# Optimization experiments

Measured on AMD Instinct MI355X. Metric: run time of the kernel, lower is better.

Reference implementation:

```python
import jax, jax.numpy as jnp
import numpy as np

N = 50000
E = 800000
IN = 256
OUT = 32
H1 = 8
NEG_SLOPE = 0.2


def setup_inputs() -> dict:
    key = jax.random.key(0)
    ks = jax.random.split(key, 12)
    x = jax.random.normal(ks[0], (N, IN), dtype=jnp.float32)
    src = jax.random.randint(ks[1], (E,), 0, N, dtype=jnp.int32)
    dst = jax.random.randint(ks[2], (E,), 0, N, dtype=jnp.int32)
    s1 = 1.0 / np.sqrt(IN)
    s2 = 1.0 / np.sqrt(H1 * OUT)
    # layer 1 (8 heads, residual = Identity since IN == H1*OUT)
    W1 = jax.random.normal(ks[3], (IN, H1 * OUT), dtype=jnp.float32) * s1
    al1 = jax.random.normal(ks[4], (H1, OUT), dtype=jnp.float32) * s1
    ar1 = jax.random.normal(ks[5], (H1, OUT), dtype=jnp.float32) * s1
    b1 = jnp.zeros((H1 * OUT,), dtype=jnp.float32)
    # layer 2 (1 head, residual = Linear since H1*OUT != OUT)
    W2 = jax.random.normal(ks[6], (H1 * OUT, OUT), dtype=jnp.float32) * s2
    al2 = jax.random.normal(ks[7], (1, OUT), dtype=jnp.float32) * s2
    ar2 = jax.random.normal(ks[8], (1, OUT), dtype=jnp.float32) * s2
    resW2 = jax.random.normal(ks[9], (H1 * OUT, OUT), dtype=jnp.float32) * s2
    b2 = jnp.zeros((OUT,), dtype=jnp.float32)
    return {"x": x, "src": src, "dst": dst, "W1": W1, "al1": al1, "ar1": ar1,
            "b1": b1, "W2": W2, "al2": al2, "ar2": ar2, "resW2": resW2, "b2": b2}


def gat_layer(x, src, dst, W, al, ar, bias, heads, out_feats, res_fn):
    # x: (N, in). feat: (N, H, D)
    feat = (x @ W).reshape(N, heads, out_feats)
    el = jnp.sum(feat * al[None], axis=-1)  # (N, H)
    er = jnp.sum(feat * ar[None], axis=-1)  # (N, H)
    e = jax.nn.leaky_relu(el[src] + er[dst], NEG_SLOPE)  # (E, H)
    # edge softmax over incoming edges of each destination node
    emax = jax.ops.segment_max(e, dst, num_segments=N)  # (N, H)
    ee = jnp.exp(e - emax[dst])
    esum = jax.ops.segment_sum(ee, dst, num_segments=N)  # (N, H)
    a = ee / esum[dst]  # (E, H)
    # gather-multiply-scatter-add aggregation
    msg = feat[src] * a[..., None]  # (E, H, D)
    rst = jax.ops.segment_sum(msg, dst, num_segments=N)  # (N, H, D)
    rst = rst + res_fn(x)
    rst = rst + bias.reshape(1, heads, out_feats)
    return rst


def reference(x, src, dst, W1, al1, ar1, b1, W2, al2, ar2, resW2, b2):
    # layer 1: 8 heads, residual Identity (IN == H1*OUT)
    y = gat_layer(x, src, dst, W1, al1, ar1, b1, H1, OUT,
                  lambda h: h.reshape(N, H1, OUT))
    y = jax.nn.relu(y).reshape(N, H1 * OUT)
    # layer 2: 1 head, residual Linear projection
    y = gat_layer(y, src, dst, W2, al2, ar2, b2, 1, OUT,
                  lambda h: (h @ resW2).reshape(N, 1, OUT))
    return y
```

## Files before the change

kernel.cpp:

```cpp
#include <hip/hip_runtime.h>
#include <hip/hip_bf16.h>
#include <hip/hip_fp8.h>

#define N_NODES 50000
#define M_PAD   50048
#define N_EDGES 800000
#define NEG_SLOPE 0.2f

#define SCAN_BLK 256
#define SCAN_NB ((N_NODES + SCAN_BLK - 1) / SCAN_BLK)
#define EPT 8
#define HIST_BLOCKS 391
#define GHALF 782
#define MEGA_T (HIST_BLOCKS + GHALF)
#define MEGA_PRIME 577ull

typedef __attribute__((ext_vector_type(8))) short bf16x8;
typedef __attribute__((ext_vector_type(4))) float f32x4;
typedef __attribute__((ext_vector_type(2))) float f32x2;

__device__ __forceinline__ unsigned short f2bf(float f) {
    unsigned u = __float_as_uint(f);
    u += 0x7FFFu + ((u >> 16) & 1u);
    return (unsigned short)(u >> 16);
}
__device__ __forceinline__ float bf2f(unsigned short h) {
    return __uint_as_float(((unsigned)h) << 16);
}

#if __has_builtin(__builtin_amdgcn_cvt_pk_f32_fp8)
__device__ __forceinline__ f32x2 fp8pk_lo(unsigned int p) { return __builtin_amdgcn_cvt_pk_f32_fp8(p, false); }
__device__ __forceinline__ f32x2 fp8pk_hi(unsigned int p) { return __builtin_amdgcn_cvt_pk_f32_fp8(p, true); }
#else
__device__ __forceinline__ float fp82f_s(unsigned char b) {
    __hip_fp8_e4m3 t; t.__x = (__hip_fp8_storage_t)b; return (float)t;
}
__device__ __forceinline__ f32x2 fp8pk_lo(unsigned int p) {
    f32x2 r; r.x = fp82f_s(p & 0xff); r.y = fp82f_s((p >> 8) & 0xff); return r;
}
__device__ __forceinline__ f32x2 fp8pk_hi(unsigned int p) {
    f32x2 r; r.x = fp82f_s((p >> 16) & 0xff); r.y = fp82f_s(p >> 24); return r;
}
#endif

#if __has_builtin(__builtin_amdgcn_cvt_pk_fp8_f32)
__device__ __forceinline__ unsigned int fp8enc2(float a, float b) {
    return (unsigned int)__builtin_amdgcn_cvt_pk_fp8_f32(a, b, 0, false);
}
#else
__device__ __forceinline__ unsigned int fp8enc2(float a, float b) {
    __hip_fp8_e4m3 ta(a), tb(b);
    return (unsigned int)ta.__x | ((unsigned int)tb.__x << 8);
}
#endif


__global__ __launch_bounds__(256) void k_trans(const float* __restrict__ W1, const float* __restrict__ W2,
                                               const float* __restrict__ resW2, const float* __restrict__ x,
                                               unsigned short* __restrict__ W1T, unsigned short* __restrict__ W2T,
                                               unsigned short* __restrict__ xb, int* __restrict__ deg) {
    int flat = blockIdx.y * 10 + blockIdx.x;
    for (int i = flat * 256 + threadIdx.x; i < N_NODES; i += 800 * 256) deg[i] = 0;

    if (blockIdx.y < 8) {
        __shared__ unsigned short tile[32][33];
        int bx = blockIdx.x;
        const float* in;
        unsigned short* out;
        int Nn, n0;
        if (bx < 8)      { in = W1;    out = W1T;            Nn = 256; n0 = bx * 32; }
        else if (bx == 8){ in = W2;    out = W2T;            Nn = 32;  n0 = 0; }
        else             { in = resW2; out = W2T + 32 * 256; Nn = 32;  n0 = 0; }
        int k0 = blockIdx.y * 32;
        int tx = threadIdx.x & 31, ty = threadIdx.x >> 5;
        #pragma unroll
        for (int r = 0; r < 4; ++r) {
            int k = k0 + ty + r * 8;
            tile[ty + r * 8][tx] = f2bf(in[(size_t)k * Nn + n0 + tx]);
        }
        __syncthreads();
        #pragma unroll
        for (int r = 0; r < 4; ++r) {
            int n = ty + r * 8;
            out[(size_t)(n0 + n) * 256 + k0 + tx] = tile[tx][n];
        }
    } else {
        int xid = flat - 80;
        const size_t NCHUNK = (size_t)M_PAD * 256 / 8;
        for (size_t c = (size_t)xid * 256 + threadIdx.x; c < NCHUNK; c += (size_t)720 * 256) {
            size_t base = c * 8;
            float4 a = make_float4(0.f, 0.f, 0.f, 0.f), b = a;
            if (base < (size_t)N_NODES * 256) {
                a = *(const float4*)(x + base);
                b = *(const float4*)(x + base + 4);
            }
            ushort4 h0, h1;
            h0.x = f2bf(a.x); h0.y = f2bf(a.y); h0.z = f2bf(a.z); h0.w = f2bf(a.w);
            h1.x = f2bf(b.x); h1.y = f2bf(b.y); h1.z = f2bf(b.z); h1.w = f2bf(b.w);
            *(ushort4*)(xb + base) = h0;
            *(ushort4*)(xb + base + 4) = h1;
        }
    }
}


__device__ __forceinline__ void gemm1_half(int g, int bn0,
                                           const unsigned short* __restrict__ xb,
                                           const unsigned short* __restrict__ BT,
                                           const float* __restrict__ al1, const float* __restrict__ ar1,
                                           unsigned char* __restrict__ Cb8,
                                           float* __restrict__ el1, float* __restrict__ er1) {
    const int t = threadIdx.x;
    const int bm0 = g * 64;
    const int wave = t >> 6, lane = t & 63;
    const int wm = (wave & 1) * 32, wn = (wave >> 1) * 64;
    const int lm = lane & 15, quad = lane >> 4;

    f32x4 acc[2][4];
    #pragma unroll
    for (int i = 0; i < 2; ++i)
        #pragma unroll
        for (int j = 0; j < 4; ++j)
            #pragma unroll
            for (int r = 0; r < 4; ++r) acc[i][j][r] = 0.f;

    const unsigned short* bp[4];
    const unsigned short* ap[2];
    #pragma unroll
    for (int i = 0; i < 4; ++i)
        bp[i] = BT + (size_t)(bn0 + wn + i * 16 + lm) * 256 + quad * 8;
    #pragma unroll
    for (int i = 0; i < 2; ++i)
        ap[i] = xb + (size_t)(bm0 + wm + i * 16 + lm) * 256 + quad * 8;

    bf16x8 nb[4], na[2];
    #pragma unroll
    for (int i = 0; i < 4; ++i) nb[i] = *(const bf16x8*)(bp[i]);
    #pragma unroll
    for (int i = 0; i < 2; ++i) na[i] = *(const bf16x8*)(ap[i]);

    #pragma unroll
    for (int k0 = 0; k0 < 256; k0 += 32) {
        bf16x8 cb[4], ca[2];
        #pragma unroll
        for (int i = 0; i < 4; ++i) cb[i] = nb[i];
        #pragma unroll
        for (int i = 0; i < 2; ++i) ca[i] = na[i];
        if (k0 + 32 < 256) {
            #pragma unroll
            for (int i = 0; i < 4; ++i) nb[i] = *(const bf16x8*)(bp[i] + k0 + 32);
            #pragma unroll
            for (int i = 0; i < 2; ++i) na[i] = *(const bf16x8*)(ap[i] + k0 + 32);
        }
        #pragma unroll
        for (int mi = 0; mi < 2; ++mi)
            #pragma unroll
            for (int ni = 0; ni < 4; ++ni)
                acc[mi][ni] = __builtin_amdgcn_mfma_f32_16x16x32_bf16(ca[mi], cb[ni], acc[mi][ni], 0, 0, 0);
    }

    #pragma unroll
    for (int mi = 0; mi < 2; ++mi) {
        #pragma unroll
        for (int ni = 0; ni < 4; ++ni) {
            int col = bn0 + wn + ni * 16 + lm;
            int row0 = bm0 + wm + mi * 16 + quad * 4;
            unsigned int p01 = fp8enc2(acc[mi][ni][0], acc[mi][ni][1]);
            unsigned int p23 = fp8enc2(acc[mi][ni][2], acc[mi][ni][3]);
            Cb8[(size_t)(row0 + 0) * 256 + col] = (unsigned char)(p01 & 0xff);
            Cb8[(size_t)(row0 + 1) * 256 + col] = (unsigned char)((p01 >> 8) & 0xff);
            Cb8[(size_t)(row0 + 2) * 256 + col] = (unsigned char)(p23 & 0xff);
            Cb8[(size_t)(row0 + 3) * 256 + col] = (unsigned char)((p23 >> 8) & 0xff);
        }
    }
    float alv[4], arv[4];
    #pragma unroll
    for (int ni = 0; ni < 4; ++ni) {
        int colg = bn0 + wn + ni * 16 + lm;
        alv[ni] = al1[colg];
        arv[ni] = ar1[colg];
    }
    int head0 = (bn0 + wn) >> 5;
    #pragma unroll
    for (int gg = 0; gg < 2; ++gg) {
        #pragma unroll
        for (int mi = 0; mi < 2; ++mi) {
            #pragma unroll
            for (int r = 0; r < 4; ++r) {
                float pel = acc[mi][2 * gg][r] * alv[2 * gg] + acc[mi][2 * gg + 1][r] * alv[2 * gg + 1];
                float per = acc[mi][2 * gg][r] * arv[2 * gg] + acc[mi][2 * gg + 1][r] * arv[2 * gg + 1];
                #pragma unroll
                for (int m = 1; m <= 8; m <<= 1) {
                    pel += __shfl_xor(pel, m, 64);
                    per += __shfl_xor(per, m, 64);
                }
                if (lm == 0) {
                    int row = bm0 + wm + mi * 16 + quad * 4 + r;
                    el1[row * 8 + head0 + gg] = pel;
                    er1[row * 8 + head0 + gg] = per;
                }
            }
        }
    }
}


__global__ __launch_bounds__(256) void k_mega1(const int* __restrict__ dst, int* __restrict__ deg,
                                               int* __restrict__ rank,
                                               const unsigned short* __restrict__ xb,
                                               const unsigned short* __restrict__ BT,
                                               const float* __restrict__ al1, const float* __restrict__ ar1,
                                               unsigned char* __restrict__ Cb8,
                                               float* __restrict__ el1, float* __restrict__ er1) {
    unsigned vb = (unsigned)(((unsigned long long)blockIdx.x * MEGA_PRIME) % MEGA_T);
    if (vb < HIST_BLOCKS) {
        int base = vb * (256 * EPT) + threadIdx.x;
        int dv[EPT];
        #pragma unroll
        for (int q = 0; q < EPT; ++q) {
            int i = base + q * 256;
            dv[q] = (i < N_EDGES) ? dst[i] : -1;
        }
        #pragma unroll
        for (int q = 0; q < EPT; ++q) {
            if (dv[q] >= 0) rank[base + q * 256] = atomicAdd(&deg[dv[q]], 1);
        }
        return;
    }
    gemm1_half(vb - HIST_BLOCKS, 0, xb, BT, al1, ar1, Cb8, el1, er1);
}


__global__ __launch_bounds__(256) void k_mega2(const int* __restrict__ src, const int* __restrict__ dst,
                                               const int* __restrict__ rowoff, const int* __restrict__ rank,
                                               int* __restrict__ csr_src,
                                               const unsigned short* __restrict__ xb,
                                               const unsigned short* __restrict__ BT,
                                               const float* __restrict__ al1, const float* __restrict__ ar1,
                                               unsigned char* __restrict__ Cb8,
                                               float* __restrict__ el1, float* __restrict__ er1) {
    unsigned vb = (unsigned)(((unsigned long long)blockIdx.x * MEGA_PRIME) % MEGA_T);
    if (vb < HIST_BLOCKS) {
        int base = vb * (256 * EPT) + threadIdx.x;
        int sv[EPT], dv[EPT], rk[EPT];
        #pragma unroll
        for (int q = 0; q < EPT; ++q) {
            int i = base + q * 256;
            if (i < N_EDGES) { sv[q] = src[i]; dv[q] = dst[i]; rk[q] = rank[i]; }
            else dv[q] = -1;
        }
        int ro[EPT];
        #pragma unroll
        for (int q = 0; q < EPT; ++q) {
            if (dv[q] >= 0) ro[q] = rowoff[dv[q]];
        }
        #pragma unroll
        for (int q = 0; q < EPT; ++q) {
            if (dv[q] >= 0) csr_src[ro[q] + rk[q]] = sv[q];
        }
        return;
    }
    gemm1_half(vb - HIST_BLOCKS, 128, xb, BT, al1, ar1, Cb8, el1, er1);
}


__global__ __launch_bounds__(SCAN_BLK) void k_scan1(const int* __restrict__ deg,
                                                    int* __restrict__ rowoff,
                                                    int* __restrict__ bsum) {
    __shared__ int s[SCAN_BLK];
    int i = blockIdx.x * SCAN_BLK + threadIdx.x;
    int v = (i < N_NODES) ? deg[i] : 0;
    s[threadIdx.x] = v;
    __syncthreads();
    for (int off = 1; off < SCAN_BLK; off <<= 1) {
        int t = (threadIdx.x >= off) ? s[threadIdx.x - off] : 0;
        __syncthreads();
        s[threadIdx.x] += t;
        __syncthreads();
    }
    if (i < N_NODES) rowoff[i] = s[threadIdx.x];
    if (threadIdx.x == SCAN_BLK - 1) bsum[blockIdx.x] = s[SCAN_BLK - 1];
}

__global__ __launch_bounds__(SCAN_BLK) void k_scan3(const int* __restrict__ deg,
                                                    int* __restrict__ rowoff,
                                                    const int* __restrict__ bsum) {
    __shared__ int red[4];
    int t = threadIdx.x;
    int part = 0;
    for (int i = t; i < (int)blockIdx.x; i += SCAN_BLK) part += bsum[i];
    #pragma unroll
    for (int m = 1; m <= 32; m <<= 1) part += __shfl_xor(part, m, 64);
    if ((t & 63) == 0) red[t >> 6] = part;
    __syncthreads();
    if (t == 0) red[0] = red[0] + red[1] + red[2] + red[3];
    __syncthreads();
    int off = red[0];
    int i = blockIdx.x * SCAN_BLK + t;
    if (i < N_NODES) rowoff[i] = rowoff[i] - deg[i] + off;
    if (i == 0) rowoff[N_NODES] = N_EDGES;
}


__global__ __launch_bounds__(256) void k_agg1(const unsigned char* __restrict__ feat8,
                                              const float* __restrict__ el1, const float* __restrict__ er1,
                                              const unsigned short* __restrict__ xb, const float* __restrict__ b1,
                                              const int* __restrict__ rowoff, const int* __restrict__ csr_src,
                                              unsigned short* __restrict__ y_b) {
    int v = (blockIdx.x * 256 + threadIdx.x) >> 6;
    int lane = threadIdx.x & 63;
    if (v >= M_PAD) return;
    int c0 = lane * 4;
    if (v >= N_NODES) {
        ushort4 z = {0, 0, 0, 0};
        *(ushort4*)(y_b + (size_t)v * 256 + c0) = z;
        return;
    }
    int h = lane >> 3;
    float er = er1[v * 8 + h];
    float ax = 0.f, ay = 0.f, az = 0.f, aw = 0.f, wsum = 0.f;
    int s = rowoff[v], e = rowoff[v + 1];
    int j = s;
    for (; j + 7 < e; j += 8) {
        int u[8];
        #pragma unroll
        for (int q = 0; q < 8; ++q) u[q] = csr_src[j + q];
        float tt[8];
        #pragma unroll
        for (int q = 0; q < 8; ++q) tt[q] = el1[u[q] * 8 + h] + er;
        unsigned int hv[8];
        #pragma unroll
        for (int q = 0; q < 8; ++q) hv[q] = *(const unsigned int*)(feat8 + (size_t)u[q] * 256 + c0);
        #pragma unroll
        for (int q = 0; q < 8; ++q) {
            float tq = tt[q] > 0.f ? tt[q] : NEG_SLOPE * tt[q];
            float w = __expf(tq);
            wsum += w;
            f32x2 lo = fp8pk_lo(hv[q]);
            f32x2 hi = fp8pk_hi(hv[q]);
            ax += w * lo.x; ay += w * lo.y; az += w * hi.x; aw += w * hi.y;
        }
    }
    for (; j + 3 < e; j += 4) {
        int u[4];
        #pragma unroll
        for (int q = 0; q < 4; ++q) u[q] = csr_src[j + q];
        float tt[4];
        #pragma unroll
        for (int q = 0; q < 4; ++q) tt[q] = el1[u[q] * 8 + h] + er;
        unsigned int hv[4];
        #pragma unroll
        for (int q = 0; q < 4; ++q) hv[q] = *(const unsigned int*)(feat8 + (size_t)u[q] * 256 + c0);
        #pragma unroll
        for (int q = 0; q < 4; ++q) {
            float tq = tt[q] > 0.f ? tt[q] : NEG_SLOPE * tt[q];
            float w = __expf(tq);
            wsum += w;
            f32x2 lo = fp8pk_lo(hv[q]);
            f32x2 hi = fp8pk_hi(hv[q]);
            ax += w * lo.x; ay += w * lo.y; az += w * hi.x; aw += w * hi.y;
        }
    }
    for (; j < e; ++j) {
        int u = csr_src[j];
        float t = el1[u * 8 + h] + er;
        unsigned int hh = *(const unsigned int*)(feat8 + (size_t)u * 256 + c0);
        t = t > 0.f ? t : NEG_SLOPE * t;
        float w = __expf(t);
        wsum += w;
        f32x2 lo = fp8pk_lo(hh);
        f32x2 hi = fp8pk_hi(hh);
        ax += w * lo.x; ay += w * lo.y; az += w * hi.x; aw += w * hi.y;
    }
    float inv = (e > s) ? 1.f / wsum : 0.f;
    ushort4 rh = *(const ushort4*)(xb + (size_t)v * 256 + c0);
    float4 bb = *(const float4*)(b1 + c0);
    ushort4 o;
    o.x = f2bf(fmaxf(ax * inv + bf2f(rh.x) + bb.x, 0.f));
    o.y = f2bf(fmaxf(ay * inv + bf2f(rh.y) + bb.y, 0.f));
    o.z = f2bf(fmaxf(az * inv + bf2f(rh.z) + bb.z, 0.f));
    o.w = f2bf(fmaxf(aw * inv + bf2f(rh.w) + bb.w, 0.f));
    *(ushort4*)(y_b + (size_t)v * 256 + c0) = o;
}


__global__ __launch_bounds__(256) void k_gemm2f(const unsigned short* __restrict__ Ab,
                                                const unsigned short* __restrict__ BT,
                                                const float* __restrict__ al2, const float* __restrict__ ar2,
                                                unsigned short* __restrict__ feat2b, float* __restrict__ res2,
                                                float* __restrict__ el2, float* __restrict__ er2) {
    const int t = threadIdx.x;
    const int bm0 = blockIdx.x * 64;
    const int wave = t >> 6, lane = t & 63;
    const int wm = (wave & 1) * 32, wn = (wave >> 1) * 32;
    const int lm = lane & 15, quad = lane >> 4;

    f32x4 acc[2][2];
    #pragma unroll
    for (int i = 0; i < 2; ++i)
        #pragma unroll
        for (int j = 0; j < 2; ++j)
            #pragma unroll
            for (int r = 0; r < 4; ++r) acc[i][j][r] = 0.f;

    const unsigned short* bp[2];
    const unsigned short* ap[2];
    #pragma unroll
    for (int i = 0; i < 2; ++i) {
        bp[i] = BT + (size_t)(wn + i * 16 + lm) * 256 + quad * 8;
        ap[i] = Ab + (size_t)(bm0 + wm + i * 16 + lm) * 256 + quad * 8;
    }

    bf16x8 nb[2], na[2];
    #pragma unroll
    for (int i = 0; i < 2; ++i) { nb[i] = *(const bf16x8*)(bp[i]); na[i] = *(const bf16x8*)(ap[i]); }

    #pragma unroll
    for (int k0 = 0; k0 < 256; k0 += 32) {
        bf16x8 cb[2], ca[2];
        #pragma unroll
        for (int i = 0; i < 2; ++i) { cb[i] = nb[i]; ca[i] = na[i]; }
        if (k0 + 32 < 256) {
            #pragma unroll
            for (int i = 0; i < 2; ++i) {
                nb[i] = *(const bf16x8*)(bp[i] + k0 + 32);
                na[i] = *(const bf16x8*)(ap[i] + k0 + 32);
            }
        }
        #pragma unroll
        for (int mi = 0; mi < 2; ++mi)
            #pragma unroll
            for (int ni = 0; ni < 2; ++ni)
                acc[mi][ni] = __builtin_amdgcn_mfma_f32_16x16x32_bf16(ca[mi], cb[ni], acc[mi][ni], 0, 0, 0);
    }

    #pragma unroll
    for (int mi = 0; mi < 2; ++mi) {
        #pragma unroll
        for (int ni = 0; ni < 2; ++ni) {
            int col = wn + ni * 16 + lm;
            #pragma unroll
            for (int r = 0; r < 4; ++r) {
                int row = bm0 + wm + mi * 16 + quad * 4 + r;
                float val = acc[mi][ni][r];
                if (col < 32) feat2b[(size_t)row * 32 + col] = f2bf(val);
                else          res2[(size_t)row * 32 + col - 32] = val;
            }
        }
    }
    if (wn == 0) {
        float alv[2], arv[2];
        #pragma unroll
        for (int ni = 0; ni < 2; ++ni) {
            alv[ni] = al2[ni * 16 + lm];
            arv[ni] = ar2[ni * 16 + lm];
        }
        #pragma unroll
        for (int mi = 0; mi < 2; ++mi) {
            #pragma unroll
            for (int r = 0; r < 4; ++r) {
                float pel = acc[mi][0][r] * alv[0] + acc[mi][1][r] * alv[1];
                float per = acc[mi][0][r] * arv[0] + acc[mi][1][r] * arv[1];
                #pragma unroll
                for (int m = 1; m <= 8; m <<= 1) {
                    pel += __shfl_xor(pel, m, 64);
                    per += __shfl_xor(per, m, 64);
                }
                if (lm == 0) {
                    int row = bm0 + wm + mi * 16 + quad * 4 + r;
                    el2[row] = pel;
                    er2[row] = per;
                }
            }
        }
    }
}


__global__ __launch_bounds__(256) void k_agg2(const unsigned short* __restrict__ feat2b,
                                              const float* __restrict__ el2, const float* __restrict__ er2,
                                              const float* __restrict__ res2, const float* __restrict__ b2,
                                              const int* __restrict__ rowoff, const int* __restrict__ csr_src,
                                              float* __restrict__ out) {
    int g = blockIdx.x * 256 + threadIdx.x;
    int v = g >> 5;
    int c = g & 31;
    if (v >= N_NODES) return;
    float er = er2[v];
    float acc = 0.f, wsum = 0.f;
    int s = rowoff[v], e = rowoff[v + 1];
    int j = s;
    for (; j + 3 < e; j += 4) {
        int u[4];
        #pragma unroll
        for (int q = 0; q < 4; ++q) u[q] = csr_src[j + q];
        float tt[4];
        #pragma unroll
        for (int q = 0; q < 4; ++q) tt[q] = el2[u[q]] + er;
        unsigned short fv[4];
        #pragma unroll
        for (int q = 0; q < 4; ++q) fv[q] = feat2b[(size_t)u[q] * 32 + c];
        #pragma unroll
        for (int q = 0; q < 4; ++q) {
            float tq = tt[q] > 0.f ? tt[q] : NEG_SLOPE * tt[q];
            float w = __expf(tq);
            wsum += w;
            acc += w * bf2f(fv[q]);
        }
    }
    for (; j < e; ++j) {
        int u = csr_src[j];
        float t = el2[u] + er;
        t = t > 0.f ? t : NEG_SLOPE * t;
        float w = __expf(t);
        wsum += w;
        acc += w * bf2f(feat2b[(size_t)u * 32 + c]);
    }
    float inv = (e > s) ? 1.f / wsum : 0.f;
    out[(size_t)v * 32 + c] = acc * inv + res2[(size_t)v * 32 + c] + b2[c];
}


extern "C" void kernel_launch(void* const* d_in, const int* in_sizes, int n_in,
                              void* d_out, int out_size, void* d_ws, size_t ws_size,
                              hipStream_t stream) {
    const float* x     = (const float*)d_in[0];
    const int*   src   = (const int*)d_in[1];
    const int*   dst   = (const int*)d_in[2];
    const float* W1    = (const float*)d_in[3];
    const float* al1   = (const float*)d_in[4];
    const float* ar1   = (const float*)d_in[5];
    const float* b1    = (const float*)d_in[6];
    const float* W2    = (const float*)d_in[7];
    const float* al2   = (const float*)d_in[8];
    const float* ar2   = (const float*)d_in[9];
    const float* resW2 = (const float*)d_in[10];
    const float* b2    = (const float*)d_in[11];
    float* out = (float*)d_out;

    char* ws = (char*)d_ws;
    size_t off = 0;
    auto alloc = [&](size_t bytes) {
        void* p = ws + off;
        off += (bytes + 255) & ~(size_t)255;
        return p;
    };
    unsigned short* xb     = (unsigned short*)alloc((size_t)M_PAD * 256 * 2);
    unsigned char*  feat8  = (unsigned char*)alloc((size_t)M_PAD * 256);
    unsigned short* y_b    = (unsigned short*)alloc((size_t)M_PAD * 256 * 2);
    unsigned short* W1T    = (unsigned short*)alloc((size_t)256 * 256 * 2);
    unsigned short* W2T    = (unsigned short*)alloc((size_t)64 * 256 * 2);
    unsigned short* feat2b = (unsigned short*)alloc((size_t)M_PAD * 32 * 2);
    float* res2   = (float*)alloc((size_t)M_PAD * 32 * 4);
    float* el1    = (float*)alloc((size_t)M_PAD * 8 * 4);
    float* er1    = (float*)alloc((size_t)M_PAD * 8 * 4);
    float* el2    = (float*)alloc((size_t)M_PAD * 4);
    float* er2    = (float*)alloc((size_t)M_PAD * 4);
    int*   deg    = (int*)alloc((size_t)N_NODES * 4);
    int*   rank   = (int*)alloc((size_t)N_EDGES * 4);
    int*   rowoff = (int*)alloc((size_t)(N_NODES + 1) * 4);
    int*   bsum   = (int*)alloc((size_t)SCAN_NB * 4);
    int*   csr    = (int*)alloc((size_t)N_EDGES * 4);
    (void)ws_size;

    k_trans<<<dim3(10, 80), 256, 0, stream>>>(W1, W2, resW2, x, W1T, W2T, xb, deg);

    k_mega1<<<MEGA_T, 256, 0, stream>>>(dst, deg, rank, xb, W1T, al1, ar1, feat8, el1, er1);

    k_scan1<<<SCAN_NB, SCAN_BLK, 0, stream>>>(deg, rowoff, bsum);
    k_scan3<<<SCAN_NB, SCAN_BLK, 0, stream>>>(deg, rowoff, bsum);

    k_mega2<<<MEGA_T, 256, 0, stream>>>(src, dst, rowoff, rank, csr, xb, W1T, al1, ar1, feat8, el1, er1);

    k_agg1<<<(M_PAD * 64) / 256, 256, 0, stream>>>(feat8, el1, er1, xb, b1, rowoff, csr, y_b);

    k_gemm2f<<<M_PAD / 64, 256, 0, stream>>>(y_b, W2T, al2, ar2, feat2b, res2, el2, er2);
    k_agg2<<<(N_NODES * 32) / 256, 256, 0, stream>>>(feat2b, el2, er2, res2, b2, rowoff, csr, out);
}
```

Measured before the change: 280.2 us.

## Split GEMM1 into 64-column tiles and share edge weights across lanes in aggregation

```diff
diff --git a/kernel.cpp b/kernel.cpp
--- a/kernel.cpp
+++ b/kernel.cpp
@@ -11,9 +11,9 @@
 #define SCAN_NB ((N_NODES + SCAN_BLK - 1) / SCAN_BLK)
 #define EPT 8
 #define HIST_BLOCKS 391
-#define GHALF 782
-#define MEGA_T (HIST_BLOCKS + GHALF)
-#define MEGA_PRIME 577ull
+#define GEMM_BLOCKS 1564
+#define MEGA_T (HIST_BLOCKS + GEMM_BLOCKS)
+#define MEGA_PRIME 997ull
 
 typedef __attribute__((ext_vector_type(8))) short bf16x8;
 typedef __attribute__((ext_vector_type(4))) float f32x4;
@@ -104,65 +104,61 @@
 }
 
 
-__device__ __forceinline__ void gemm1_half(int g, int bn0,
-                                           const unsigned short* __restrict__ xb,
-                                           const unsigned short* __restrict__ BT,
-                                           const float* __restrict__ al1, const float* __restrict__ ar1,
-                                           unsigned char* __restrict__ Cb8,
-                                           float* __restrict__ el1, float* __restrict__ er1) {
+__device__ __forceinline__ void gemm1_64(int gm, int bn0,
+                                         const unsigned short* __restrict__ xb,
+                                         const unsigned short* __restrict__ BT,
+                                         const float* __restrict__ al1, const float* __restrict__ ar1,
+                                         unsigned char* __restrict__ Cb8,
+                                         float* __restrict__ el1, float* __restrict__ er1) {
     const int t = threadIdx.x;
-    const int bm0 = g * 64;
+    const int bm0 = gm * 64;
     const int wave = t >> 6, lane = t & 63;
-    const int wm = (wave & 1) * 32, wn = (wave >> 1) * 64;
+    const int wm = (wave & 1) * 32, wn = (wave >> 1) * 32;
     const int lm = lane & 15, quad = lane >> 4;
 
-    f32x4 acc[2][4];
+    f32x4 acc[2][2];
     #pragma unroll
     for (int i = 0; i < 2; ++i)
         #pragma unroll
-        for (int j = 0; j < 4; ++j)
+        for (int j = 0; j < 2; ++j)
             #pragma unroll
             for (int r = 0; r < 4; ++r) acc[i][j][r] = 0.f;
 
-    const unsigned short* bp[4];
+    const unsigned short* bp[2];
     const unsigned short* ap[2];
     #pragma unroll
-    for (int i = 0; i < 4; ++i)
+    for (int i = 0; i < 2; ++i) {
         bp[i] = BT + (size_t)(bn0 + wn + i * 16 + lm) * 256 + quad * 8;
-    #pragma unroll
-    for (int i = 0; i < 2; ++i)
         ap[i] = xb + (size_t)(bm0 + wm + i * 16 + lm) * 256 + quad * 8;
-
-    bf16x8 nb[4], na[2];
-    #pragma unroll
-    for (int i = 0; i < 4; ++i) nb[i] = *(const bf16x8*)(bp[i]);
-    #pragma unroll
-    for (int i = 0; i < 2; ++i) na[i] = *(const bf16x8*)(ap[i]);
+    }
+
+    bf16x8 nb[2], na[2];
+    #pragma unroll
+    for (int i = 0; i < 2; ++i) { nb[i] = *(const bf16x8*)(bp[i]); na[i] = *(const bf16x8*)(ap[i]); }
 
     #pragma unroll
     for (int k0 = 0; k0 < 256; k0 += 32) {
-        bf16x8 cb[4], ca[2];
-        #pragma unroll
-        for (int i = 0; i < 4; ++i) cb[i] = nb[i];
-        #pragma unroll
-        for (int i = 0; i < 2; ++i) ca[i] = na[i];
+        bf16x8 cb[2], ca[2];
+        #pragma unroll
+        for (int i = 0; i < 2; ++i) { cb[i] = nb[i]; ca[i] = na[i]; }
         if (k0 + 32 < 256) {
             #pragma unroll
-            for (int i = 0; i < 4; ++i) nb[i] = *(const bf16x8*)(bp[i] + k0 + 32);
-            #pragma unroll
-            for (int i = 0; i < 2; ++i) na[i] = *(const bf16x8*)(ap[i] + k0 + 32);
+            for (int i = 0; i < 2; ++i) {
+                nb[i] = *(const bf16x8*)(bp[i] + k0 + 32);
+                na[i] = *(const bf16x8*)(ap[i] + k0 + 32);
+            }
         }
         #pragma unroll
         for (int mi = 0; mi < 2; ++mi)
             #pragma unroll
-            for (int ni = 0; ni < 4; ++ni)
+            for (int ni = 0; ni < 2; ++ni)
                 acc[mi][ni] = __builtin_amdgcn_mfma_f32_16x16x32_bf16(ca[mi], cb[ni], acc[mi][ni], 0, 0, 0);
     }
 
     #pragma unroll
     for (int mi = 0; mi < 2; ++mi) {
         #pragma unroll
-        for (int ni = 0; ni < 4; ++ni) {
+        for (int ni = 0; ni < 2; ++ni) {
             int col = bn0 + wn + ni * 16 + lm;
             int row0 = bm0 + wm + mi * 16 + quad * 4;
             unsigned int p01 = fp8enc2(acc[mi][ni][0], acc[mi][ni][1]);
@@ -173,32 +169,29 @@
             Cb8[(size_t)(row0 + 3) * 256 + col] = (unsigned char)((p23 >> 8) & 0xff);
         }
     }
-    float alv[4], arv[4];
-    #pragma unroll
-    for (int ni = 0; ni < 4; ++ni) {
+    int head = (bn0 + wn) >> 5;
+    float alv[2], arv[2];
+    #pragma unroll
+    for (int ni = 0; ni < 2; ++ni) {
         int colg = bn0 + wn + ni * 16 + lm;
         alv[ni] = al1[colg];
         arv[ni] = ar1[colg];
     }
-    int head0 = (bn0 + wn) >> 5;
-    #pragma unroll
-    for (int gg = 0; gg < 2; ++gg) {
-        #pragma unroll
-        for (int mi = 0; mi < 2; ++mi) {
-            #pragma unroll
-            for (int r = 0; r < 4; ++r) {
-                float pel = acc[mi][2 * gg][r] * alv[2 * gg] + acc[mi][2 * gg + 1][r] * alv[2 * gg + 1];
-                float per = acc[mi][2 * gg][r] * arv[2 * gg] + acc[mi][2 * gg + 1][r] * arv[2 * gg + 1];
-                #pragma unroll
-                for (int m = 1; m <= 8; m <<= 1) {
-                    pel += __shfl_xor(pel, m, 64);
-                    per += __shfl_xor(per, m, 64);
-                }
-                if (lm == 0) {
-                    int row = bm0 + wm + mi * 16 + quad * 4 + r;
-                    el1[row * 8 + head0 + gg] = pel;
-                    er1[row * 8 + head0 + gg] = per;
-                }
+    #pragma unroll
+    for (int mi = 0; mi < 2; ++mi) {
+        #pragma unroll
+        for (int r = 0; r < 4; ++r) {
+            float pel = acc[mi][0][r] * alv[0] + acc[mi][1][r] * alv[1];
+            float per = acc[mi][0][r] * arv[0] + acc[mi][1][r] * arv[1];
+            #pragma unroll
+            for (int m = 1; m <= 8; m <<= 1) {
+                pel += __shfl_xor(pel, m, 64);
+                per += __shfl_xor(per, m, 64);
+            }
+            if (lm == 0) {
+                int row = bm0 + wm + mi * 16 + quad * 4 + r;
+                el1[row * 8 + head] = pel;
+                er1[row * 8 + head] = per;
             }
         }
     }
@@ -227,7 +220,8 @@
         }
         return;
     }
-    gemm1_half(vb - HIST_BLOCKS, 0, xb, BT, al1, ar1, Cb8, el1, er1);
+    int g = vb - HIST_BLOCKS;
+    gemm1_64(g >> 1, (g & 1) * 64, xb, BT, al1, ar1, Cb8, el1, er1);
 }
 
 
@@ -260,7 +254,8 @@
         }
         return;
     }
-    gemm1_half(vb - HIST_BLOCKS, 128, xb, BT, al1, ar1, Cb8, el1, er1);
+    int g = vb - HIST_BLOCKS;
+    gemm1_64(g >> 1, 128 + (g & 1) * 64, xb, BT, al1, ar1, Cb8, el1, er1);
 }
 
 
@@ -317,23 +312,45 @@
         return;
     }
     int h = lane >> 3;
-    float er = er1[v * 8 + h];
+    float er  = er1[v * 8 + h];
+    float erc = er1[v * 8 + (lane & 7)];
     float ax = 0.f, ay = 0.f, az = 0.f, aw = 0.f, wsum = 0.f;
     int s = rowoff[v], e = rowoff[v + 1];
     int j = s;
     for (; j + 7 < e; j += 8) {
+        int um = csr_src[j + (lane >> 3)];
+        float elv = el1[um * 8 + (lane & 7)];
         int u[8];
         #pragma unroll
-        for (int q = 0; q < 8; ++q) u[q] = csr_src[j + q];
-        float tt[8];
-        #pragma unroll
-        for (int q = 0; q < 8; ++q) tt[q] = el1[u[q] * 8 + h] + er;
+        for (int q = 0; q < 8; ++q) u[q] = __shfl(um, q * 8);
         unsigned int hv[8];
         #pragma unroll
         for (int q = 0; q < 8; ++q) hv[q] = *(const unsigned int*)(feat8 + (size_t)u[q] * 256 + c0);
+        float tq = elv + erc;
+        tq = fmaxf(tq, NEG_SLOPE * tq);
+        float wv = __expf(tq);
         #pragma unroll
         for (int q = 0; q < 8; ++q) {
-            float tq = tt[q] > 0.f ? tt[q] : NEG_SLOPE * tt[q];
+            float w = __shfl(wv, q * 8 + h);
+            wsum += w;
+            f32x2 lo = fp8pk_lo(hv[q]);
+            f32x2 hi = fp8pk_hi(hv[q]);
+            ax += w * lo.x; ay += w * lo.y; az += w * hi.x; aw += w * hi.y;
+        }
+    }
+    for (; j + 3 < e; j += 4) {
+        int u[4];
+        #pragma unroll
+        for (int q = 0; q < 4; ++q) u[q] = csr_src[j + q];
+        float tt[4];
+        #pragma unroll
+        for (int q = 0; q < 4; ++q) tt[q] = el1[u[q] * 8 + h] + er;
+        unsigned int hv[4];
+        #pragma unroll
+        for (int q = 0; q < 4; ++q) hv[q] = *(const unsigned int*)(feat8 + (size_t)u[q] * 256 + c0);
+        #pragma unroll
+        for (int q = 0; q < 4; ++q) {
+            float tq = fmaxf(tt[q], NEG_SLOPE * tt[q]);
             float w = __expf(tq);
             wsum += w;
             f32x2 lo = fp8pk_lo(hv[q]);
@@ -341,31 +358,11 @@
             ax += w * lo.x; ay += w * lo.y; az += w * hi.x; aw += w * hi.y;
         }
     }
-    for (; j + 3 < e; j += 4) {
-        int u[4];
-        #pragma unroll
-        for (int q = 0; q < 4; ++q) u[q] = csr_src[j + q];
-        float tt[4];
-        #pragma unroll
-        for (int q = 0; q < 4; ++q) tt[q] = el1[u[q] * 8 + h] + er;
-        unsigned int hv[4];
-        #pragma unroll
-        for (int q = 0; q < 4; ++q) hv[q] = *(const unsigned int*)(feat8 + (size_t)u[q] * 256 + c0);
-        #pragma unroll
-        for (int q = 0; q < 4; ++q) {
-            float tq = tt[q] > 0.f ? tt[q] : NEG_SLOPE * tt[q];
-            float w = __expf(tq);
-            wsum += w;
-            f32x2 lo = fp8pk_lo(hv[q]);
-            f32x2 hi = fp8pk_hi(hv[q]);
-            ax += w * lo.x; ay += w * lo.y; az += w * hi.x; aw += w * hi.y;
-        }
-    }
     for (; j < e; ++j) {
         int u = csr_src[j];
         float t = el1[u * 8 + h] + er;
         unsigned int hh = *(const unsigned int*)(feat8 + (size_t)u * 256 + c0);
-        t = t > 0.f ? t : NEG_SLOPE * t;
+        t = fmaxf(t, NEG_SLOPE * t);
         float w = __expf(t);
         wsum += w;
         f32x2 lo = fp8pk_lo(hh);
@@ -502,7 +499,7 @@
         for (int q = 0; q < 4; ++q) fv[q] = feat2b[(size_t)u[q] * 32 + c];
         #pragma unroll
         for (int q = 0; q < 4; ++q) {
-            float tq = tt[q] > 0.f ? tt[q] : NEG_SLOPE * tt[q];
+            float tq = fmaxf(tt[q], NEG_SLOPE * tt[q]);
             float w = __expf(tq);
             wsum += w;
             acc += w * bf2f(fv[q]);
@@ -511,7 +508,7 @@
     for (; j < e; ++j) {
         int u = csr_src[j];
         float t = el2[u] + er;
-        t = t > 0.f ? t : NEG_SLOPE * t;
+        t = fmaxf(t, NEG_SLOPE * t);
         float w = __expf(t);
         wsum += w;
         acc += w * bf2f(feat2b[(size_t)u * 32 + c]);
```

Result: slower. 287.9 us (+2.8%).

## Build CSR via bucketed shared-memory counting sort, drop scan kernels

Applied to the files above, without the earlier changes.

```diff
diff --git a/kernel.cpp b/kernel.cpp
--- a/kernel.cpp
+++ b/kernel.cpp
@@ -7,13 +7,16 @@
 #define N_EDGES 800000
 #define NEG_SLOPE 0.2f
 
-#define SCAN_BLK 256
-#define SCAN_NB ((N_NODES + SCAN_BLK - 1) / SCAN_BLK)
 #define EPT 8
-#define HIST_BLOCKS 391
+#define BKA 391
+#define NBUCK 256
+#define NPB 196
+#define SEGCAP 40
 #define GHALF 782
-#define MEGA_T (HIST_BLOCKS + GHALF)
-#define MEGA_PRIME 577ull
+#define MEGA1_T (BKA + GHALF)
+#define MEGA1_PRIME 577ull
+#define MEGA2_T (NBUCK + GHALF)
+#define MEGA2_PRIME 521ull
 
 typedef __attribute__((ext_vector_type(8))) short bf16x8;
 typedef __attribute__((ext_vector_type(4))) float f32x4;
@@ -58,9 +61,9 @@
 __global__ __launch_bounds__(256) void k_trans(const float* __restrict__ W1, const float* __restrict__ W2,
                                                const float* __restrict__ resW2, const float* __restrict__ x,
                                                unsigned short* __restrict__ W1T, unsigned short* __restrict__ W2T,
-                                               unsigned short* __restrict__ xb, int* __restrict__ deg) {
+                                               unsigned short* __restrict__ xb, unsigned int* __restrict__ btot) {
     int flat = blockIdx.y * 10 + blockIdx.x;
-    for (int i = flat * 256 + threadIdx.x; i < N_NODES; i += 800 * 256) deg[i] = 0;
+    if (flat == 0) btot[threadIdx.x] = 0;
 
     if (blockIdx.y < 8) {
         __shared__ unsigned short tile[32][33];
@@ -205,100 +208,111 @@
 }
 
 
-__global__ __launch_bounds__(256) void k_mega1(const int* __restrict__ dst, int* __restrict__ deg,
-                                               int* __restrict__ rank,
+__global__ __launch_bounds__(256) void k_mega1(const int* __restrict__ src, const int* __restrict__ dst,
+                                               uint2* __restrict__ seg, unsigned int* __restrict__ cnt,
+                                               unsigned int* __restrict__ btot,
                                                const unsigned short* __restrict__ xb,
                                                const unsigned short* __restrict__ BT,
                                                const float* __restrict__ al1, const float* __restrict__ ar1,
                                                unsigned char* __restrict__ Cb8,
                                                float* __restrict__ el1, float* __restrict__ er1) {
-    unsigned vb = (unsigned)(((unsigned long long)blockIdx.x * MEGA_PRIME) % MEGA_T);
-    if (vb < HIST_BLOCKS) {
+    __shared__ unsigned int lcnt[NBUCK];
+    unsigned vb = (unsigned)(((unsigned long long)blockIdx.x * MEGA1_PRIME) % MEGA1_T);
+    if (vb < BKA) {
+        lcnt[threadIdx.x] = 0;
+        __syncthreads();
         int base = vb * (256 * EPT) + threadIdx.x;
-        int dv[EPT];
+        int sv[EPT], dv[EPT], bk[EPT], lr[EPT];
         #pragma unroll
         for (int q = 0; q < EPT; ++q) {
             int i = base + q * 256;
-            dv[q] = (i < N_EDGES) ? dst[i] : -1;
+            if (i < N_EDGES) { sv[q] = src[i]; dv[q] = dst[i]; }
+            else dv[q] = -1;
         }
         #pragma unroll
         for (int q = 0; q < EPT; ++q) {
-            if (dv[q] >= 0) rank[base + q * 256] = atomicAdd(&deg[dv[q]], 1);
+            if (dv[q] >= 0) {
+                bk[q] = (int)((unsigned)dv[q] / NPB);
+                lr[q] = atomicAdd(&lcnt[bk[q]], 1u);
+            }
+        }
+        __syncthreads();
+        cnt[vb * NBUCK + threadIdx.x] = lcnt[threadIdx.x];
+        if (lcnt[threadIdx.x] > 0) atomicAdd(&btot[threadIdx.x], lcnt[threadIdx.x]);
+        #pragma unroll
+        for (int q = 0; q < EPT; ++q) {
+            if (dv[q] >= 0 && lr[q] < SEGCAP) {
+                size_t slot = ((size_t)bk[q] * BKA + vb) * SEGCAP + lr[q];
+                seg[slot] = make_uint2((unsigned)sv[q], (unsigned)dv[q] - (unsigned)bk[q] * NPB);
+            }
         }
         return;
     }
-    gemm1_half(vb - HIST_BLOCKS, 0, xb, BT, al1, ar1, Cb8, el1, er1);
-}
-
-
-__global__ __launch_bounds__(256) void k_mega2(const int* __restrict__ src, const int* __restrict__ dst,
-                                               const int* __restrict__ rowoff, const int* __restrict__ rank,
-                                               int* __restrict__ csr_src,
+    gemm1_half(vb - BKA, 0, xb, BT, al1, ar1, Cb8, el1, er1);
+}
+
+
+__global__ __launch_bounds__(256) void k_mega2(const uint2* __restrict__ seg, const unsigned int* __restrict__ cnt,
+                                               const unsigned int* __restrict__ btot,
+                                               int* __restrict__ rowoff, int* __restrict__ csr_src,
                                                const unsigned short* __restrict__ xb,
                                                const unsigned short* __restrict__ BT,
                                                const float* __restrict__ al1, const float* __restrict__ ar1,
                                                unsigned char* __restrict__ Cb8,
                                                float* __restrict__ el1, float* __restrict__ er1) {
-    unsigned vb = (unsigned)(((unsigned long long)blockIdx.x * MEGA_PRIME) % MEGA_T);
-    if (vb < HIST_BLOCKS) {
-        int base = vb * (256 * EPT) + threadIdx.x;
-        int sv[EPT], dv[EPT], rk[EPT];
-        #pragma unroll
-        for (int q = 0; q < EPT; ++q) {
-            int i = base + q * 256;
-            if (i < N_EDGES) { sv[q] = src[i]; dv[q] = dst[i]; rk[q] = rank[i]; }
-            else dv[q] = -1;
-        }
-        int ro[EPT];
-        #pragma unroll
-        for (int q = 0; q < EPT; ++q) {
-            if (dv[q] >= 0) ro[q] = rowoff[dv[q]];
-        }
-        #pragma unroll
-        for (int q = 0; q < EPT; ++q) {
-            if (dv[q] >= 0) csr_src[ro[q] + rk[q]] = sv[q];
+    __shared__ unsigned int hist[NPB];
+    __shared__ unsigned int cursor[NPB];
+    __shared__ unsigned int red[256];
+    unsigned vb = (unsigned)(((unsigned long long)blockIdx.x * MEGA2_PRIME) % MEGA2_T);
+    if (vb < NBUCK) {
+        int b = (int)vb;
+        int t = threadIdx.x;
+        if (t < NPB) hist[t] = 0;
+        red[t] = (t < b) ? btot[t] : 0;
+        __syncthreads();
+        #pragma unroll
+        for (int off = 128; off > 0; off >>= 1) {
+            if (t < off) red[t] += red[t + off];
+            __syncthreads();
+        }
+        unsigned int base = red[0];
+        __syncthreads();
+        for (int s = t; s < BKA; s += 256) {
+            unsigned int c = cnt[s * NBUCK + b];
+            const uint2* sp = seg + ((size_t)b * BKA + s) * SEGCAP;
+            for (unsigned int j = 0; j < c; ++j) {
+                atomicAdd(&hist[sp[j].y], 1u);
+            }
+        }
+        __syncthreads();
+        red[t] = (t < NPB) ? hist[t] : 0;
+        __syncthreads();
+        for (int off = 1; off < 256; off <<= 1) {
+            unsigned int val = (t >= off) ? red[t - off] : 0;
+            __syncthreads();
+            red[t] += val;
+            __syncthreads();
+        }
+        if (t < NPB) {
+            unsigned int excl = red[t] - hist[t];
+            cursor[t] = excl;
+            int v = b * NPB + t;
+            if (v < N_NODES) rowoff[v] = (int)(base + excl);
+        }
+        if (b == NBUCK - 1 && t == 0) rowoff[N_NODES] = N_EDGES;
+        __syncthreads();
+        for (int s = t; s < BKA; s += 256) {
+            unsigned int c = cnt[s * NBUCK + b];
+            const uint2* sp = seg + ((size_t)b * BKA + s) * SEGCAP;
+            for (unsigned int j = 0; j < c; ++j) {
+                uint2 eg = sp[j];
+                unsigned int r = atomicAdd(&cursor[eg.y], 1u);
+                csr_src[base + r] = (int)eg.x;
+            }
         }
         return;
     }
-    gemm1_half(vb - HIST_BLOCKS, 128, xb, BT, al1, ar1, Cb8, el1, er1);
-}
-
-
-__global__ __launch_bounds__(SCAN_BLK) void k_scan1(const int* __restrict__ deg,
-                                                    int* __restrict__ rowoff,
-                                                    int* __restrict__ bsum) {
-    __shared__ int s[SCAN_BLK];
-    int i = blockIdx.x * SCAN_BLK + threadIdx.x;
-    int v = (i < N_NODES) ? deg[i] : 0;
-    s[threadIdx.x] = v;
-    __syncthreads();
-    for (int off = 1; off < SCAN_BLK; off <<= 1) {
-        int t = (threadIdx.x >= off) ? s[threadIdx.x - off] : 0;
-        __syncthreads();
-        s[threadIdx.x] += t;
-        __syncthreads();
-    }
-    if (i < N_NODES) rowoff[i] = s[threadIdx.x];
-    if (threadIdx.x == SCAN_BLK - 1) bsum[blockIdx.x] = s[SCAN_BLK - 1];
-}
-
-__global__ __launch_bounds__(SCAN_BLK) void k_scan3(const int* __restrict__ deg,
-                                                    int* __restrict__ rowoff,
-                                                    const int* __restrict__ bsum) {
-    __shared__ int red[4];
-    int t = threadIdx.x;
-    int part = 0;
-    for (int i = t; i < (int)blockIdx.x; i += SCAN_BLK) part += bsum[i];
-    #pragma unroll
-    for (int m = 1; m <= 32; m <<= 1) part += __shfl_xor(part, m, 64);
-    if ((t & 63) == 0) red[t >> 6] = part;
-    __syncthreads();
-    if (t == 0) red[0] = red[0] + red[1] + red[2] + red[3];
-    __syncthreads();
-    int off = red[0];
-    int i = blockIdx.x * SCAN_BLK + t;
-    if (i < N_NODES) rowoff[i] = rowoff[i] - deg[i] + off;
-    if (i == 0) rowoff[N_NODES] = N_EDGES;
+    gemm1_half(vb - NBUCK, 128, xb, BT, al1, ar1, Cb8, el1, er1);
 }
 
 
@@ -317,23 +331,45 @@
         return;
     }
     int h = lane >> 3;
-    float er = er1[v * 8 + h];
+    float er  = er1[v * 8 + h];
+    float erc = er1[v * 8 + (lane & 7)];
     float ax = 0.f, ay = 0.f, az = 0.f, aw = 0.f, wsum = 0.f;
     int s = rowoff[v], e = rowoff[v + 1];
     int j = s;
     for (; j + 7 < e; j += 8) {
+        int um = csr_src[j + (lane >> 3)];
+        float elv = el1[um * 8 + (lane & 7)];
         int u[8];
         #pragma unroll
-        for (int q = 0; q < 8; ++q) u[q] = csr_src[j + q];
-        float tt[8];
-        #pragma unroll
-        for (int q = 0; q < 8; ++q) tt[q] = el1[u[q] * 8 + h] + er;
+        for (int q = 0; q < 8; ++q) u[q] = __shfl(um, q * 8);
         unsigned int hv[8];
         #pragma unroll
         for (int q = 0; q < 8; ++q) hv[q] = *(const unsigned int*)(feat8 + (size_t)u[q] * 256 + c0);
+        float tq = elv + erc;
+        tq = fmaxf(tq, NEG_SLOPE * tq);
+        float wv = __expf(tq);
         #pragma unroll
         for (int q = 0; q < 8; ++q) {
-            float tq = tt[q] > 0.f ? tt[q] : NEG_SLOPE * tt[q];
+            float w = __shfl(wv, q * 8 + h);
+            wsum += w;
+            f32x2 lo = fp8pk_lo(hv[q]);
+            f32x2 hi = fp8pk_hi(hv[q]);
+            ax += w * lo.x; ay += w * lo.y; az += w * hi.x; aw += w * hi.y;
+        }
+    }
+    for (; j + 3 < e; j += 4) {
+        int u[4];
+        #pragma unroll
+        for (int q = 0; q < 4; ++q) u[q] = csr_src[j + q];
+        float tt[4];
+        #pragma unroll
+        for (int q = 0; q < 4; ++q) tt[q] = el1[u[q] * 8 + h] + er;
+        unsigned int hv[4];
+        #pragma unroll
+        for (int q = 0; q < 4; ++q) hv[q] = *(const unsigned int*)(feat8 + (size_t)u[q] * 256 + c0);
+        #pragma unroll
+        for (int q = 0; q < 4; ++q) {
+            float tq = fmaxf(tt[q], NEG_SLOPE * tt[q]);
             float w = __expf(tq);
             wsum += w;
             f32x2 lo = fp8pk_lo(hv[q]);
@@ -341,31 +377,11 @@
             ax += w * lo.x; ay += w * lo.y; az += w * hi.x; aw += w * hi.y;
         }
     }
-    for (; j + 3 < e; j += 4) {
-        int u[4];
-        #pragma unroll
-        for (int q = 0; q < 4; ++q) u[q] = csr_src[j + q];
-        float tt[4];
-        #pragma unroll
-        for (int q = 0; q < 4; ++q) tt[q] = el1[u[q] * 8 + h] + er;
-        unsigned int hv[4];
-        #pragma unroll
-        for (int q = 0; q < 4; ++q) hv[q] = *(const unsigned int*)(feat8 + (size_t)u[q] * 256 + c0);
-        #pragma unroll
-        for (int q = 0; q < 4; ++q) {
-            float tq = tt[q] > 0.f ? tt[q] : NEG_SLOPE * tt[q];
-            float w = __expf(tq);
-            wsum += w;
-            f32x2 lo = fp8pk_lo(hv[q]);
-            f32x2 hi = fp8pk_hi(hv[q]);
-            ax += w * lo.x; ay += w * lo.y; az += w * hi.x; aw += w * hi.y;
-        }
-    }
     for (; j < e; ++j) {
         int u = csr_src[j];
         float t = el1[u * 8 + h] + er;
         unsigned int hh = *(const unsigned int*)(feat8 + (size_t)u * 256 + c0);
-        t = t > 0.f ? t : NEG_SLOPE * t;
+        t = fmaxf(t, NEG_SLOPE * t);
         float w = __expf(t);
         wsum += w;
         f32x2 lo = fp8pk_lo(hh);
@@ -502,7 +518,7 @@
         for (int q = 0; q < 4; ++q) fv[q] = feat2b[(size_t)u[q] * 32 + c];
         #pragma unroll
         for (int q = 0; q < 4; ++q) {
-            float tq = tt[q] > 0.f ? tt[q] : NEG_SLOPE * tt[q];
+            float tq = fmaxf(tt[q], NEG_SLOPE * tt[q]);
             float w = __expf(tq);
             wsum += w;
             acc += w * bf2f(fv[q]);
@@ -511,7 +527,7 @@
     for (; j < e; ++j) {
         int u = csr_src[j];
         float t = el2[u] + er;
-        t = t > 0.f ? t : NEG_SLOPE * t;
+        t = fmaxf(t, NEG_SLOPE * t);
         float w = __expf(t);
         wsum += w;
         acc += w * bf2f(feat2b[(size_t)u * 32 + c]);
@@ -556,21 +572,18 @@
     float* er1    = (float*)alloc((size_t)M_PAD * 8 * 4);
     float* el2    = (float*)alloc((size_t)M_PAD * 4);
     float* er2    = (float*)alloc((size_t)M_PAD * 4);
-    int*   deg    = (int*)alloc((size_t)N_NODES * 4);
-    int*   rank   = (int*)alloc((size_t)N_EDGES * 4);
     int*   rowoff = (int*)alloc((size_t)(N_NODES + 1) * 4);
-    int*   bsum   = (int*)alloc((size_t)SCAN_NB * 4);
     int*   csr    = (int*)alloc((size_t)N_EDGES * 4);
+    uint2* seg    = (uint2*)alloc((size_t)NBUCK * BKA * SEGCAP * 8);
+    unsigned int* cnt  = (unsigned int*)alloc((size_t)BKA * NBUCK * 4);
+    unsigned int* btot = (unsigned int*)alloc((size_t)NBUCK * 4);
     (void)ws_size;
 
-    k_trans<<<dim3(10, 80), 256, 0, stream>>>(W1, W2, resW2, x, W1T, W2T, xb, deg);
-
-    k_mega1<<<MEGA_T, 256, 0, stream>>>(dst, deg, rank, xb, W1T, al1, ar1, feat8, el1, er1);
-
-    k_scan1<<<SCAN_NB, SCAN_BLK, 0, stream>>>(deg, rowoff, bsum);
-    k_scan3<<<SCAN_NB, SCAN_BLK, 0, stream>>>(deg, rowoff, bsum);
-
-    k_mega2<<<MEGA_T, 256, 0, stream>>>(src, dst, rowoff, rank, csr, xb, W1T, al1, ar1, feat8, el1, er1);
+    k_trans<<<dim3(10, 80), 256, 0, stream>>>(W1, W2, resW2, x, W1T, W2T, xb, btot);
+
+    k_mega1<<<MEGA1_T, 256, 0, stream>>>(src, dst, seg, cnt, btot, xb, W1T, al1, ar1, feat8, el1, er1);
+
+    k_mega2<<<MEGA2_T, 256, 0, stream>>>(seg, cnt, btot, rowoff, csr, xb, W1T, al1, ar1, feat8, el1, er1);
 
     k_agg1<<<(M_PAD * 64) / 256, 256, 0, stream>>>(feat8, el1, er1, xb, b1, rowoff, csr, y_b);
 
```

New measurement: 265.3 us. 1.06x faster.
